# Kernel optimization log

Hardware: AMD Instinct MI355X
Metric: run time of the kernel (lower is better)

## Reference

```python
import jax, jax.numpy as jnp
import numpy as np

N_NODES = 50000
N_EDGES = 800000
DIM_NODE = 64
DIM_EDGE = 32
OUT_DIM = 64
NEG_SLOPE = 0.01  # torch F.leaky_relu default; module's negative_slope arg is unused in forward


def setup_inputs() -> dict:
    key = jax.random.key(0)
    k = jax.random.split(key, 8)
    d_in1 = 2 * DIM_NODE + DIM_EDGE  # 160
    d_h = 2 * DIM_NODE               # 128
    # Kaiming-uniform-ish init scale like torch Linear
    def lin(kw, kb, fan_in, fan_out):
        bound = 1.0 / np.sqrt(fan_in)
        W = jax.random.uniform(kw, (fan_out, fan_in), minval=-bound, maxval=bound, dtype=jnp.float32)
        b = jax.random.uniform(kb, (fan_out,), minval=-bound, maxval=bound, dtype=jnp.float32)
        return W, b
    W1, b1 = lin(k[0], k[1], d_in1, d_h)
    W2, b2 = lin(k[2], k[3], d_h, OUT_DIM)
    x = jax.random.normal(k[4], (N_NODES, DIM_NODE), dtype=jnp.float32)
    edge_index = jax.random.randint(k[5], (2, N_EDGES), 0, N_NODES, dtype=jnp.int64 if jax.config.jax_enable_x64 else jnp.int32).astype(jnp.int32)
    edge_attr = jax.random.normal(k[6], (N_EDGES, DIM_EDGE), dtype=jnp.float32)
    return {"x": x, "edge_index": edge_index, "edge_attr": edge_attr,
            "W1": W1, "b1": b1, "W2": W2, "b2": b2}


def reference(x, edge_index, edge_attr, W1, b1, W2, b2):
    # gather endpoint node features per edge: [E, dim_node]
    x_i = x[edge_index[0]]
    x_j = x[edge_index[1]]
    mask = jnp.concatenate([x_i, x_j, edge_attr], axis=-1)  # [E, 2*dn+de]
    h = jnp.dot(mask, W1.T) + b1                             # [E, 2*dn]
    h = jnp.where(h >= 0, h, NEG_SLOPE * h)                  # leaky_relu (slope 0.01)
    out = jnp.dot(h, W2.T) + b2                              # [E, out_dim]
    return out
```

## Files before the change

### kernel.cpp

```cpp
#include <hip/hip_runtime.h>
#include <stdint.h>
#include <stddef.h>


typedef short short8 __attribute__((ext_vector_type(8)));
typedef float f32x4 __attribute__((ext_vector_type(4)));

__device__ __forceinline__ short f2bf(float f) {
  union { float f; unsigned u; } v; v.f = f;
  unsigned r = (v.u + 0x7fffu + ((v.u >> 16) & 1u)) >> 16;
  return (short)r;
}

__device__ __forceinline__ short8 cvt8(const float* __restrict__ p) {
  f32x4 a = *(const f32x4*)p;
  f32x4 b = *(const f32x4*)(p + 4);
  short8 r;
  r[0] = f2bf(a[0]); r[1] = f2bf(a[1]); r[2] = f2bf(a[2]); r[3] = f2bf(a[3]);
  r[4] = f2bf(b[0]); r[5] = f2bf(b[1]); r[6] = f2bf(b[2]); r[7] = f2bf(b[3]);
  return r;
}

__global__ __launch_bounds__(256, 2)
void edge_mlp(const float* __restrict__ x, const int* __restrict__ ei,
              const float* __restrict__ ea, const float* __restrict__ W1,
              const float* __restrict__ b1, const float* __restrict__ W2,
              const float* __restrict__ b2, float* __restrict__ out,
              int E, int ntiles)
{
  __shared__ short sW1[128 * 168];
  __shared__ short sH[4][32 * 40];

  const int tid  = threadIdx.x;
  const int lane = tid & 63;
  const int wave = tid >> 6;
  const int m    = lane & 15;
  const int quad = lane >> 4;

  for (int i = tid; i < 128 * 160; i += 256) {
    int n = i / 160;
    int k = i - n * 160;
    sW1[n * 168 + k] = f2bf(W1[i]);
  }

  short8 w2f[4][4];
#pragma unroll
  for (int ot = 0; ot < 4; ++ot)
#pragma unroll
    for (int c = 0; c < 4; ++c)
      w2f[ot][c] = cvt8(W2 + (size_t)(ot * 16 + m) * 128 + c * 32 + quad * 8);

  float b1v[8], b2v[4];
#pragma unroll
  for (int nt = 0; nt < 8; ++nt) b1v[nt] = b1[nt * 16 + m];
#pragma unroll
  for (int ot = 0; ot < 4; ++ot) b2v[ot] = b2[ot * 16 + m];

  __syncthreads();

  short* sHw = sH[wave];

  for (int t = blockIdx.x; t < ntiles; t += gridDim.x) {
    const int ebase = t * 128 + wave * 32;

    short8 a1[2][5];
#pragma unroll
    for (int mt = 0; mt < 2; ++mt) {
      int e = ebase + mt * 16 + m;
      e = (e < E) ? e : (E - 1);
      const int i0 = ei[e];
      const int i1 = ei[E + e];
      const float* r0 = x + (size_t)i0 * 64 + quad * 8;
      const float* r1 = x + (size_t)i1 * 64 + quad * 8;
      a1[mt][0] = cvt8(r0);
      a1[mt][1] = cvt8(r0 + 32);
      a1[mt][2] = cvt8(r1);
      a1[mt][3] = cvt8(r1 + 32);
      a1[mt][4] = cvt8(ea + (size_t)e * 32 + quad * 8);
    }

    f32x4 acc2[2][4];
#pragma unroll
    for (int mt = 0; mt < 2; ++mt)
#pragma unroll
      for (int ot = 0; ot < 4; ++ot) {
        f32x4 z = { b2v[ot], b2v[ot], b2v[ot], b2v[ot] };
        acc2[mt][ot] = z;
      }

#pragma unroll
    for (int c = 0; c < 4; ++c) {
#pragma unroll
      for (int sub = 0; sub < 2; ++sub) {
        const int nt = c * 2 + sub;
        f32x4 h0 = { b1v[nt], b1v[nt], b1v[nt], b1v[nt] };
        f32x4 h1 = h0;
#pragma unroll
        for (int kt = 0; kt < 5; ++kt) {
          short8 bf = *(const short8*)&sW1[(nt * 16 + m) * 168 + kt * 32 + quad * 8];
          h0 = __builtin_amdgcn_mfma_f32_16x16x32_bf16(a1[0][kt], bf, h0, 0, 0, 0);
          h1 = __builtin_amdgcn_mfma_f32_16x16x32_bf16(a1[1][kt], bf, h1, 0, 0, 0);
        }
#pragma unroll
        for (int r = 0; r < 4; ++r) {
          float v0 = h0[r]; v0 = (v0 >= 0.0f) ? v0 : 0.01f * v0;
          float v1 = h1[r]; v1 = (v1 >= 0.0f) ? v1 : 0.01f * v1;
          sHw[(quad * 4 + r) * 40 + sub * 16 + m]      = f2bf(v0);
          sHw[(16 + quad * 4 + r) * 40 + sub * 16 + m] = f2bf(v1);
        }
      }
#pragma unroll
      for (int mt = 0; mt < 2; ++mt) {
        short8 a2 = *(const short8*)&sHw[(mt * 16 + m) * 40 + quad * 8];
#pragma unroll
        for (int ot = 0; ot < 4; ++ot)
          acc2[mt][ot] = __builtin_amdgcn_mfma_f32_16x16x32_bf16(a2, w2f[ot][c], acc2[mt][ot], 0, 0, 0);
      }
    }

#pragma unroll
    for (int mt = 0; mt < 2; ++mt)
#pragma unroll
      for (int ot = 0; ot < 4; ++ot)
#pragma unroll
        for (int r = 0; r < 4; ++r) {
          int er = ebase + mt * 16 + quad * 4 + r;
          if (er < E) out[(size_t)er * 64 + ot * 16 + m] = acc2[mt][ot][r];
        }
  }
}

extern "C" void kernel_launch(void* const* d_in, const int* in_sizes, int n_in,
                              void* d_out, int out_size, void* d_ws, size_t ws_size,
                              hipStream_t stream) {
  const float* x  = (const float*)d_in[0];
  const int*   ei = (const int*)d_in[1];
  const float* ea = (const float*)d_in[2];
  const float* W1 = (const float*)d_in[3];
  const float* b1 = (const float*)d_in[4];
  const float* W2 = (const float*)d_in[5];
  const float* b2 = (const float*)d_in[6];
  float* out = (float*)d_out;

  const int E = in_sizes[1] / 2;
  const int ntiles = (E + 127) / 128;
  int grid = ntiles < 1250 ? ntiles : 1250;

  edge_mlp<<<grid, 256, 0, stream>>>(x, ei, ea, W1, b1, W2, b2, out, E, ntiles);
}
```

Measured before the change: 387.4 us.

## Transpose MFMA operands to keep hidden layer in registers and vectorize stores

Swaps the MFMA A/B operands so each lane holds rows of edges, which lets the leaky-ReLU hidden tile feed the second GEMM straight from registers instead of round-tripping through per-wave LDS, and lets outputs be written as contiguous float4 nontemporal stores. It also prefetches the next tile's edge indices, uses nontemporal loads for edge attributes, vectorizes the W1 staging, and moves biases to LDS. The grid changes from a fixed persistent 1250 blocks to 4 tiles per block, with launch bounds raised to 3 blocks per SM. Together these restructure the tile schedule and the register/LDS data flow. More, shorter-lived blocks each repeat the W1/W2 staging, which adds setup cost.

```diff
diff --git a/kernel.cpp b/kernel.cpp
--- a/kernel.cpp
+++ b/kernel.cpp
@@ -4,7 +4,10 @@
 
 
 typedef short short8 __attribute__((ext_vector_type(8)));
+typedef short bf4 __attribute__((ext_vector_type(4)));
 typedef float f32x4 __attribute__((ext_vector_type(4)));
+
+#define TILES_PER_BLOCK 4
 
 __device__ __forceinline__ short f2bf(float f) {
   union { float f; unsigned u; } v; v.f = f;
@@ -21,7 +24,16 @@
   return r;
 }
 
-__global__ __launch_bounds__(256, 2)
+__device__ __forceinline__ short8 cvt8_nt(const float* __restrict__ p) {
+  f32x4 a = __builtin_nontemporal_load((const f32x4*)p);
+  f32x4 b = __builtin_nontemporal_load((const f32x4*)(p + 4));
+  short8 r;
+  r[0] = f2bf(a[0]); r[1] = f2bf(a[1]); r[2] = f2bf(a[2]); r[3] = f2bf(a[3]);
+  r[4] = f2bf(b[0]); r[5] = f2bf(b[1]); r[6] = f2bf(b[2]); r[7] = f2bf(b[3]);
+  return r;
+}
+
+__global__ __launch_bounds__(256, 3)
 void edge_mlp(const float* __restrict__ x, const int* __restrict__ ei,
               const float* __restrict__ ea, const float* __restrict__ W1,
               const float* __restrict__ b1, const float* __restrict__ W2,
@@ -29,104 +41,131 @@
               int E, int ntiles)
 {
   __shared__ short sW1[128 * 168];
-  __shared__ short sH[4][32 * 40];
+  __shared__ float sB1[128];
+  __shared__ float sB2[64];
 
   const int tid  = threadIdx.x;
   const int lane = tid & 63;
   const int wave = tid >> 6;
   const int m    = lane & 15;
-  const int quad = lane >> 4;
+  const int q    = lane >> 4;
 
-  for (int i = tid; i < 128 * 160; i += 256) {
-    int n = i / 160;
-    int k = i - n * 160;
-    sW1[n * 168 + k] = f2bf(W1[i]);
+  for (int i = tid; i < 128 * 40; i += 256) {
+    int n  = i / 40;
+    int k4 = (i - n * 40) * 4;
+    f32x4 v = *(const f32x4*)(W1 + n * 160 + k4);
+    bf4 s; s[0] = f2bf(v[0]); s[1] = f2bf(v[1]); s[2] = f2bf(v[2]); s[3] = f2bf(v[3]);
+    *(bf4*)&sW1[n * 168 + k4] = s;
   }
+  if (tid < 128) sB1[tid] = b1[tid];
+  if (tid < 64)  sB2[tid] = b2[tid];
 
   short8 w2f[4][4];
 #pragma unroll
   for (int ot = 0; ot < 4; ++ot)
 #pragma unroll
-    for (int c = 0; c < 4; ++c)
-      w2f[ot][c] = cvt8(W2 + (size_t)(ot * 16 + m) * 128 + c * 32 + quad * 8);
-
-  float b1v[8], b2v[4];
-#pragma unroll
-  for (int nt = 0; nt < 8; ++nt) b1v[nt] = b1[nt * 16 + m];
-#pragma unroll
-  for (int ot = 0; ot < 4; ++ot) b2v[ot] = b2[ot * 16 + m];
+    for (int c = 0; c < 4; ++c) {
+      const float* base = W2 + (size_t)(ot * 16 + m) * 128 + c * 32 + q * 4;
+      f32x4 lo = *(const f32x4*)base;
+      f32x4 hi = *(const f32x4*)(base + 16);
+      short8 w;
+      w[0] = f2bf(lo[0]); w[1] = f2bf(lo[1]); w[2] = f2bf(lo[2]); w[3] = f2bf(lo[3]);
+      w[4] = f2bf(hi[0]); w[5] = f2bf(hi[1]); w[6] = f2bf(hi[2]); w[7] = f2bf(hi[3]);
+      w2f[ot][c] = w;
+    }
 
   __syncthreads();
 
-  short* sHw = sH[wave];
+  const int t0   = blockIdx.x * TILES_PER_BLOCK;
+  const int tend = (t0 + TILES_PER_BLOCK < ntiles) ? t0 + TILES_PER_BLOCK : ntiles;
+  if (t0 >= ntiles) return;
 
-  for (int t = blockIdx.x; t < ntiles; t += gridDim.x) {
-    const int ebase = t * 128 + wave * 32;
+  int nI0[2], nI1[2];
+  {
+    const int eb = t0 * 128 + wave * 32;
+#pragma unroll
+    for (int mt = 0; mt < 2; ++mt) {
+      int e = eb + mt * 16 + m; e = (e < E) ? e : (E - 1);
+      nI0[mt] = ei[e]; nI1[mt] = ei[E + e];
+    }
+  }
+
+  for (int t = t0; t < tend; ++t) {
+    const int eb = t * 128 + wave * 32;
+    const int cI0[2] = { nI0[0], nI0[1] };
+    const int cI1[2] = { nI1[0], nI1[1] };
+    if (t + 1 < tend) {
+      const int eb2 = eb + 128;
+#pragma unroll
+      for (int mt = 0; mt < 2; ++mt) {
+        int e = eb2 + mt * 16 + m; e = (e < E) ? e : (E - 1);
+        nI0[mt] = ei[e]; nI1[mt] = ei[E + e];
+      }
+    }
 
     short8 a1[2][5];
 #pragma unroll
     for (int mt = 0; mt < 2; ++mt) {
-      int e = ebase + mt * 16 + m;
-      e = (e < E) ? e : (E - 1);
-      const int i0 = ei[e];
-      const int i1 = ei[E + e];
-      const float* r0 = x + (size_t)i0 * 64 + quad * 8;
-      const float* r1 = x + (size_t)i1 * 64 + quad * 8;
+      int e = eb + mt * 16 + m; e = (e < E) ? e : (E - 1);
+      const float* r0 = x + (size_t)cI0[mt] * 64 + q * 8;
+      const float* r1 = x + (size_t)cI1[mt] * 64 + q * 8;
       a1[mt][0] = cvt8(r0);
       a1[mt][1] = cvt8(r0 + 32);
       a1[mt][2] = cvt8(r1);
       a1[mt][3] = cvt8(r1 + 32);
-      a1[mt][4] = cvt8(ea + (size_t)e * 32 + quad * 8);
+      a1[mt][4] = cvt8_nt(ea + (size_t)e * 32 + q * 8);
     }
 
     f32x4 acc2[2][4];
 #pragma unroll
-    for (int mt = 0; mt < 2; ++mt)
-#pragma unroll
-      for (int ot = 0; ot < 4; ++ot) {
-        f32x4 z = { b2v[ot], b2v[ot], b2v[ot], b2v[ot] };
-        acc2[mt][ot] = z;
-      }
+    for (int ot = 0; ot < 4; ++ot) {
+      f32x4 bb = *(const f32x4*)&sB2[ot * 16 + q * 4];
+      acc2[0][ot] = bb; acc2[1][ot] = bb;
+    }
 
 #pragma unroll
     for (int c = 0; c < 4; ++c) {
+      f32x4 hs[2][2];
 #pragma unroll
       for (int sub = 0; sub < 2; ++sub) {
         const int nt = c * 2 + sub;
-        f32x4 h0 = { b1v[nt], b1v[nt], b1v[nt], b1v[nt] };
-        f32x4 h1 = h0;
+        f32x4 binit = *(const f32x4*)&sB1[nt * 16 + q * 4];
+        f32x4 h0 = binit, h1 = binit;
 #pragma unroll
         for (int kt = 0; kt < 5; ++kt) {
-          short8 bf = *(const short8*)&sW1[(nt * 16 + m) * 168 + kt * 32 + quad * 8];
-          h0 = __builtin_amdgcn_mfma_f32_16x16x32_bf16(a1[0][kt], bf, h0, 0, 0, 0);
-          h1 = __builtin_amdgcn_mfma_f32_16x16x32_bf16(a1[1][kt], bf, h1, 0, 0, 0);
+          short8 wf = *(const short8*)&sW1[(nt * 16 + m) * 168 + kt * 32 + q * 8];
+          h0 = __builtin_amdgcn_mfma_f32_16x16x32_bf16(wf, a1[0][kt], h0, 0, 0, 0);
+          h1 = __builtin_amdgcn_mfma_f32_16x16x32_bf16(wf, a1[1][kt], h1, 0, 0, 0);
         }
-#pragma unroll
-        for (int r = 0; r < 4; ++r) {
-          float v0 = h0[r]; v0 = (v0 >= 0.0f) ? v0 : 0.01f * v0;
-          float v1 = h1[r]; v1 = (v1 >= 0.0f) ? v1 : 0.01f * v1;
-          sHw[(quad * 4 + r) * 40 + sub * 16 + m]      = f2bf(v0);
-          sHw[(16 + quad * 4 + r) * 40 + sub * 16 + m] = f2bf(v1);
-        }
+        hs[sub][0] = h0; hs[sub][1] = h1;
       }
 #pragma unroll
       for (int mt = 0; mt < 2; ++mt) {
-        short8 a2 = *(const short8*)&sHw[(mt * 16 + m) * 40 + quad * 8];
+        short8 hb;
+#pragma unroll
+        for (int sub = 0; sub < 2; ++sub)
+#pragma unroll
+          for (int r = 0; r < 4; ++r) {
+            float v = hs[sub][mt][r];
+            v = (v >= 0.0f) ? v : 0.01f * v;
+            hb[sub * 4 + r] = f2bf(v);
+          }
 #pragma unroll
         for (int ot = 0; ot < 4; ++ot)
-          acc2[mt][ot] = __builtin_amdgcn_mfma_f32_16x16x32_bf16(a2, w2f[ot][c], acc2[mt][ot], 0, 0, 0);
+          acc2[mt][ot] = __builtin_amdgcn_mfma_f32_16x16x32_bf16(w2f[ot][c], hb, acc2[mt][ot], 0, 0, 0);
       }
     }
 
 #pragma unroll
-    for (int mt = 0; mt < 2; ++mt)
+    for (int mt = 0; mt < 2; ++mt) {
+      int e = eb + mt * 16 + m;
+      if (e < E) {
+        float* op = out + (size_t)e * 64 + q * 4;
 #pragma unroll
-      for (int ot = 0; ot < 4; ++ot)
-#pragma unroll
-        for (int r = 0; r < 4; ++r) {
-          int er = ebase + mt * 16 + quad * 4 + r;
-          if (er < E) out[(size_t)er * 64 + ot * 16 + m] = acc2[mt][ot][r];
-        }
+        for (int ot = 0; ot < 4; ++ot)
+          __builtin_nontemporal_store(acc2[mt][ot], (f32x4*)(op + ot * 16));
+      }
+    }
   }
 }
 
@@ -144,7 +183,7 @@
 
   const int E = in_sizes[1] / 2;
   const int ntiles = (E + 127) / 128;
-  int grid = ntiles < 1250 ? ntiles : 1250;
+  const int grid = (ntiles + TILES_PER_BLOCK - 1) / TILES_PER_BLOCK;
 
   edge_mlp<<<grid, 256, 0, stream>>>(x, ei, ea, W1, b1, W2, b2, out, E, ntiles);
 }
```

After: 739.6 us. 90.9% more time.
